# Optimization experiments

Measured on AMD Instinct MI355X. Metric: run time of the kernel, lower is better.

The kernel has to match this reference:

```python
import jax, jax.numpy as jnp
import numpy as np
import math

V, T, D, H, L, B = 50257, 1024, 768, 12, 6, 2
FF = 4 * D
HD = D // H

def layernorm(x, g, b, eps=1e-5):
    mu = jnp.mean(x, axis=-1, keepdims=True)
    var = jnp.var(x, axis=-1, keepdims=True)
    return (x - mu) * jax.lax.rsqrt(var + eps) * g + b

def new_gelu(x):
    # Faithful to the (buggy) NewGelu: tanh arg = sqrt(2/pi) * 0.044715 * x**4
    c = math.sqrt(2.0 / math.pi)
    return 0.5 * x * (1.0 + jnp.tanh(c * (x * 0.044715 * jnp.power(x, 3))))

def setup_inputs() -> dict:
    key = jax.random.key(0)
    ks = jax.random.split(key, 18)
    n = lambda k, shape, s=0.02: (jax.random.normal(k, shape, dtype=jnp.float32) * s)
    return {
        "ids": jax.random.randint(ks[0], (B, T), 0, V),
        "wte": n(ks[1], (V, D)),
        "wpe": n(ks[2], (T, D)),
        "W_qkv": n(ks[3], (L, D, 3 * D)),
        "b_qkv": jnp.zeros((L, 3 * D), jnp.float32),
        "W_o": n(ks[4], (L, D, D)),
        "b_o": jnp.zeros((L, D), jnp.float32),
        "ln1_g": jnp.ones((L, D), jnp.float32),
        "ln1_b": jnp.zeros((L, D), jnp.float32),
        "W1": n(ks[5], (L, D, FF)),
        "b1": jnp.zeros((L, FF), jnp.float32),
        "W2": n(ks[6], (L, FF, D)),
        "b2": jnp.zeros((L, D), jnp.float32),
        "lnf_g": jnp.ones((D,), jnp.float32),
        "lnf_b": jnp.zeros((D,), jnp.float32),
        "W_head": n(ks[7], (D, V)),
        "b_head": jnp.zeros((V,), jnp.float32),
    }

def reference(ids, wte, wpe, W_qkv, b_qkv, W_o, b_o, ln1_g, ln1_b,
              W1, b1, W2, b2, lnf_g, lnf_b, W_head, b_head):
    t = ids.shape[1]
    x = wte[ids] + wpe[:t][None]  # [B,T,D]
    scale = 1.0 / math.sqrt(HD)
    for l in range(L):
        qkv = x @ W_qkv[l] + b_qkv[l]                 # [B,T,3D]
        q, k, v = jnp.split(qkv, 3, axis=-1)
        q = q.reshape(-1, t, H, HD).transpose(0, 2, 1, 3)  # [B,H,T,hd]
        k = k.reshape(-1, t, H, HD).transpose(0, 2, 1, 3)
        v = v.reshape(-1, t, H, HD).transpose(0, 2, 1, 3)
        # NOTE: mask buffer is all-ones in the source, so NO causal masking.
        att = jax.nn.softmax(jnp.einsum('bhqd,bhkd->bhqk', q, k) * scale, axis=-1)
        y = jnp.einsum('bhqk,bhkd->bhqd', att, v)
        y = y.transpose(0, 2, 1, 3).reshape(-1, t, D)
        y = y @ W_o[l] + b_o[l]
        x = layernorm(y, ln1_g[l], ln1_b[l]) + x      # ln1 AFTER attn, per source
        h = new_gelu(x @ W1[l] + b1[l]) @ W2[l] + b2[l]  # ln2 unused, per source
        x = h + x
    x = layernorm(x, lnf_g, lnf_b)
    logits = x @ W_head + b_head
    return logits
```

## Files before the change

kernel.cpp:

```cpp
#include <hip/hip_runtime.h>
#include <hip/hip_bf16.h>
#include <math.h>
#include <stdint.h>

#define NL 6
#define NB 2
#define ST 1024
#define ND 768
#define NH 12
#define HD 64
#define NFF 3072
#define NV 50257
#define ND3 2304
#define NM (NB * ST)

typedef short bf16x4 __attribute__((ext_vector_type(4)));
typedef short bf16x8 __attribute__((ext_vector_type(8)));
typedef float f32x4  __attribute__((ext_vector_type(4)));

typedef __attribute__((address_space(3))) void as3_void;
typedef __attribute__((address_space(1))) void as1_void;

__device__ __forceinline__ void async_copy16(const void* g, void* lds) {
  __builtin_amdgcn_global_load_lds((const as1_void*)(uintptr_t)g,
                                   (as3_void*)(uint32_t)(uintptr_t)lds,
                                   16, 0, 0);
}

__device__ __forceinline__ unsigned short f2bf(float f) {
  union { float f; uint32_t u; } v; v.f = f;
  return (unsigned short)((v.u + 0x7fffu + ((v.u >> 16) & 1u)) >> 16);
}

__device__ __forceinline__ bf16x8 frag16(const unsigned short* p) {
  return *(const bf16x8*)p;
}

template <int N>
__device__ __forceinline__ void wait_vm_barrier() {
  if constexpr (N == 8)      asm volatile("s_waitcnt vmcnt(8)\n\ts_barrier" ::: "memory");
  else if constexpr (N == 6) asm volatile("s_waitcnt vmcnt(6)\n\ts_barrier" ::: "memory");
  else if constexpr (N == 4) asm volatile("s_waitcnt vmcnt(4)\n\ts_barrier" ::: "memory");
  else                       asm volatile("s_waitcnt vmcnt(0)\n\ts_barrier" ::: "memory");
}
__device__ __forceinline__ void lgkm_barrier() {
  asm volatile("s_waitcnt lgkmcnt(0)\n\ts_barrier" ::: "memory");
}

#define MFMA(a, b, c) __builtin_amdgcn_mfma_f32_16x16x32_bf16((a), (b), (c), 0, 0, 0)

__device__ __forceinline__ float gelu_buggy(float x) {
  const float c = 0.7978845608028654f;
  float x2 = x * x;
  return 0.5f * x * (1.0f + tanhf(c * 0.044715f * x2 * x2));
}

enum { EP_QKV = 0, EP_PROJ, EP_FF1, EP_FF2, EP_HEAD };

template <int EPI, int TM, int TN, int WN, int NW, int BK>
__global__ __launch_bounds__(NW * 64)
void gemm_bt(const unsigned short* __restrict__ A,
             const unsigned short* __restrict__ BT,
             const float* __restrict__ bias,
             float* __restrict__ Cf,
             unsigned short* __restrict__ Cb,
             const float* __restrict__ resid,
             unsigned short* __restrict__ vT,
             int M, int N, int K)
{
  constexpr int WM = NW / WN;
  constexpr int FM = TM / WM / 16;
  constexpr int FN = TN / WN / 16;
  constexpr int SL = BK / 8;
  constexpr int RS = (BK == 32) ? 1 : 0;
  constexpr int RPC = 1024 / (BK * 2);
  constexpr int CA = TM / RPC / NW;
  constexpr int CB = TN / RPC / NW;
  constexpr int LPT = CA + CB;
  constexpr int KK = BK / 32;
  __shared__ __align__(16) unsigned short As[2][TM * BK];
  __shared__ __align__(16) unsigned short Bs[2][TN * BK];
  const int tid = threadIdx.x;
  const int w = tid >> 6, l = tid & 63;
  const int g = l >> 4, r = l & 15;
  const int wm = (w / WN) * (FM * 16);
  const int wn = (w % WN) * (FN * 16);

  const int nbx = gridDim.x;
  const int nwg = nbx * gridDim.y;
  int bid = blockIdx.y * nbx + blockIdx.x;
  if ((nwg & 7) == 0) bid = (bid & 7) * (nwg >> 3) + (bid >> 3);
  const int m0 = (bid % nbx) * TM, n0 = (bid / nbx) * TN;

  const int sr = l / (BK / 8);
  const int se = ((l & (SL - 1)) ^ ((sr >> RS) & (SL - 1))) * 8;
  long aoff[CA];
  long boff[CB];
#pragma unroll
  for (int c = 0; c < CA; ++c) {
    const int arow = (w * CA + c) * RPC + sr;
    aoff[c] = (long)(m0 + arow) * K + se;
  }
#pragma unroll
  for (int c = 0; c < CB; ++c) {
    int brow = n0 + (w * CB + c) * RPC + sr;
    if (brow > N - 1) brow = N - 1;
    boff[c] = (long)brow * K + se;
  }

  f32x4 acc[FM][FN] = {};

  auto stage = [&](int t, int buf) {
    const long k0 = (long)t * BK;
#pragma unroll
    for (int c = 0; c < CA; ++c)
      async_copy16(A + aoff[c] + k0, &As[buf][(w * CA + c) * 512]);
#pragma unroll
    for (int c = 0; c < CB; ++c)
      async_copy16(BT + boff[c] + k0, &Bs[buf][(w * CB + c) * 512]);
  };

  auto compute = [&](int buf) {
#pragma unroll
    for (int kk = 0; kk < KK; ++kk) {
      bf16x8 af[FM], bf[FN];
#pragma unroll
      for (int mi = 0; mi < FM; ++mi)
        af[mi] = frag16(&As[buf][(wm + mi * 16 + r) * BK +
                                 (((kk * 4 + g) ^ ((r >> RS) & (SL - 1))) * 8)]);
#pragma unroll
      for (int ni = 0; ni < FN; ++ni)
        bf[ni] = frag16(&Bs[buf][(wn + ni * 16 + r) * BK +
                                 (((kk * 4 + g) ^ ((r >> RS) & (SL - 1))) * 8)]);
      __builtin_amdgcn_s_setprio(1);
#pragma unroll
      for (int mi = 0; mi < FM; ++mi)
#pragma unroll
        for (int ni = 0; ni < FN; ++ni)
          acc[mi][ni] = MFMA(af[mi], bf[ni], acc[mi][ni]);
      __builtin_amdgcn_s_setprio(0);
    }
  };

  const int nt = K / BK;
  stage(0, 0);
  for (int t = 0; t < nt - 1; ++t) {
    stage(t + 1, (t + 1) & 1);
    wait_vm_barrier<LPT>();
    compute(t & 1);
    lgkm_barrier();
  }
  wait_vm_barrier<0>();
  compute((nt - 1) & 1);

#pragma unroll
  for (int mi = 0; mi < FM; ++mi) {
#pragma unroll
    for (int ni = 0; ni < FN; ++ni) {
      const int col = n0 + wn + ni * 16 + r;
      if (EPI == EP_HEAD && col >= N) continue;
      const float bb = bias[col];
      if (EPI == EP_QKV && col >= 2 * ND) {
        const int hv = (col - 2 * ND) >> 6, d = (col - 2 * ND) & 63;
        short4 vv;
#pragma unroll
        for (int q = 0; q < 4; ++q)
          vv[q] = (short)f2bf(acc[mi][ni][q] + bb);
        const int row = m0 + wm + mi * 16 + g * 4;
        const int bb_ = row >> 10, t4 = row & 1023;
        *(short4*)&vT[(((long)bb_ * NH + hv) * HD + d) * ST + t4] = vv;
        continue;
      }
#pragma unroll
      for (int q = 0; q < 4; ++q) {
        const int row = m0 + wm + mi * 16 + g * 4 + q;
        float v = acc[mi][ni][q] + bb;
        if constexpr (EPI == EP_QKV) {
          Cb[(long)row * N + col] = f2bf(v);
        } else if constexpr (EPI == EP_PROJ) {
          Cf[(long)row * N + col] = v;
        } else if constexpr (EPI == EP_FF1) {
          Cb[(long)row * N + col] = f2bf(gelu_buggy(v));
        } else if constexpr (EPI == EP_FF2) {
          float o = v + resid[(long)row * N + col];
          Cf[(long)row * N + col] = o;
          Cb[(long)row * N + col] = f2bf(o);
        } else {
          Cf[(long)row * N + col] = v;
        }
      }
    }
  }
}

__global__ __launch_bounds__(256)
void attn_kernel(const unsigned short* __restrict__ qkv,
                 const unsigned short* __restrict__ vT,
                 unsigned short* __restrict__ y)
{
  constexpr int LS = 72;
  __shared__ __align__(16) unsigned short Qs[64 * LS];
  __shared__ __align__(16) unsigned short Ks[64 * LS];
  __shared__ __align__(16) unsigned short Vt[64 * LS];
  __shared__ __align__(16) unsigned short Ps[64 * LS];
  const int tid = threadIdx.x;
  const int w = tid >> 6, l = tid & 63;
  const int g = l >> 4, r = l & 15;
  const int q0 = blockIdx.x * 64;
  const int b = blockIdx.y / NH, h = blockIdx.y % NH;
  const long rb = (long)b * ST;
  const long vbase = ((long)b * NH + h) * HD * ST;
  const int srow = tid >> 3, sc8 = (tid & 7) * 8;

#pragma unroll
  for (int p = 0; p < 2; ++p) {
    const int row = p * 32 + srow;
    bf16x8 v = *(const bf16x8*)&qkv[(rb + q0 + row) * ND3 + h * HD + sc8];
    *(bf16x8*)&Qs[row * LS + sc8] = v;
  }
  __syncthreads();
  bf16x8 aq[2];
#pragma unroll
  for (int kk = 0; kk < 2; ++kk)
    aq[kk] = *(const bf16x8*)&Qs[(w * 16 + r) * LS + kk * 32 + g * 8];

  float m_run[4] = {-1e30f, -1e30f, -1e30f, -1e30f};
  float l_run[4] = {0.f, 0.f, 0.f, 0.f};
  f32x4 acc_o[4] = {};

  for (int kt = 0; kt < ST / 64; ++kt) {
#pragma unroll
    for (int p = 0; p < 2; ++p) {
      const int row = p * 32 + srow;
      *(bf16x8*)&Ks[row * LS + sc8] =
          *(const bf16x8*)&qkv[(rb + kt * 64 + row) * ND3 + ND + h * HD + sc8];
      *(bf16x8*)&Vt[row * LS + sc8] =
          *(const bf16x8*)&vT[vbase + (long)row * ST + kt * 64 + sc8];
    }
    __syncthreads();

    f32x4 s_acc[4] = {};
#pragma unroll
    for (int kk = 0; kk < 2; ++kk) {
#pragma unroll
      for (int ni = 0; ni < 4; ++ni) {
        bf16x8 bk = *(const bf16x8*)&Ks[(ni * 16 + r) * LS + kk * 32 + g * 8];
        s_acc[ni] = MFMA(aq[kk], bk, s_acc[ni]);
      }
    }

    float mloc[4];
#pragma unroll
    for (int q = 0; q < 4; ++q) {
      float mx = fmaxf(fmaxf(s_acc[0][q], s_acc[1][q]), fmaxf(s_acc[2][q], s_acc[3][q]));
      mloc[q] = mx * 0.125f;
    }
#pragma unroll
    for (int mask = 1; mask < 16; mask <<= 1)
#pragma unroll
      for (int q = 0; q < 4; ++q)
        mloc[q] = fmaxf(mloc[q], __shfl_xor(mloc[q], mask, 64));

    float alpha[4], psum[4] = {0.f, 0.f, 0.f, 0.f};
#pragma unroll
    for (int q = 0; q < 4; ++q) {
      const float mn = fmaxf(m_run[q], mloc[q]);
      alpha[q] = __expf(m_run[q] - mn);
      m_run[q] = mn;
    }
#pragma unroll
    for (int ni = 0; ni < 4; ++ni)
#pragma unroll
      for (int q = 0; q < 4; ++q) {
        const float p = __expf(s_acc[ni][q] * 0.125f - m_run[q]);
        psum[q] += p;
        Ps[(w * 16 + g * 4 + q) * LS + ni * 16 + r] = f2bf(p);
      }
#pragma unroll
    for (int mask = 1; mask < 16; mask <<= 1)
#pragma unroll
      for (int q = 0; q < 4; ++q) psum[q] += __shfl_xor(psum[q], mask, 64);
#pragma unroll
    for (int q = 0; q < 4; ++q) l_run[q] = l_run[q] * alpha[q] + psum[q];
#pragma unroll
    for (int ni = 0; ni < 4; ++ni)
#pragma unroll
      for (int q = 0; q < 4; ++q) acc_o[ni][q] *= alpha[q];

    asm volatile("s_waitcnt lgkmcnt(0)" ::: "memory");
    __builtin_amdgcn_sched_barrier(0);

#pragma unroll
    for (int kk = 0; kk < 2; ++kk) {
      bf16x8 ap = *(const bf16x8*)&Ps[(w * 16 + r) * LS + kk * 32 + g * 8];
#pragma unroll
      for (int ni = 0; ni < 4; ++ni) {
        bf16x8 bv = *(const bf16x8*)&Vt[(ni * 16 + r) * LS + kk * 32 + g * 8];
        acc_o[ni] = MFMA(ap, bv, acc_o[ni]);
      }
    }
    __syncthreads();
  }

#pragma unroll
  for (int ni = 0; ni < 4; ++ni)
#pragma unroll
    for (int q = 0; q < 4; ++q) {
      const int row = q0 + w * 16 + g * 4 + q;
      const int col = h * HD + ni * 16 + r;
      y[(rb + row) * ND + col] = f2bf(acc_o[ni][q] / l_run[q]);
    }
}

template <bool RESID>
__global__ __launch_bounds__(256)
void ln_kernel(const float* __restrict__ in, const float* __restrict__ resid,
               const float* __restrict__ gamma, const float* __restrict__ beta,
               float* __restrict__ out_f, unsigned short* __restrict__ out_b)
{
  __shared__ float wred[8];
  const int row = blockIdx.x, tid = threadIdx.x;
  float v[3];
#pragma unroll
  for (int j = 0; j < 3; ++j) v[j] = in[(long)row * ND + tid + j * 256];
  float s = v[0] + v[1] + v[2];
#pragma unroll
  for (int m = 1; m < 64; m <<= 1) s += __shfl_xor(s, m, 64);
  if ((tid & 63) == 0) wred[tid >> 6] = s;
  __syncthreads();
  const float mean = (wred[0] + wred[1] + wred[2] + wred[3]) * (1.0f / ND);
  float d[3];
#pragma unroll
  for (int j = 0; j < 3; ++j) d[j] = v[j] - mean;
  float s2 = d[0] * d[0] + d[1] * d[1] + d[2] * d[2];
#pragma unroll
  for (int m = 1; m < 64; m <<= 1) s2 += __shfl_xor(s2, m, 64);
  if ((tid & 63) == 0) wred[4 + (tid >> 6)] = s2;
  __syncthreads();
  const float var = (wred[4] + wred[5] + wred[6] + wred[7]) * (1.0f / ND);
  const float rstd = rsqrtf(var + 1e-5f);
#pragma unroll
  for (int j = 0; j < 3; ++j) {
    const int c = tid + j * 256;
    float o = d[j] * rstd * gamma[c] + beta[c];
    if (RESID) o += resid[(long)row * ND + c];
    if (out_f) out_f[(long)row * ND + c] = o;
    if (out_b) out_b[(long)row * ND + c] = f2bf(o);
  }
}

__global__ __launch_bounds__(256)
void embed_kernel(const int* __restrict__ ids, const float* __restrict__ wte,
                  const float* __restrict__ wpe, float* __restrict__ x,
                  unsigned short* __restrict__ xb)
{
  const int t = blockIdx.x, tid = threadIdx.x;
  const int tok = ids[t];
  const int pos = t & (ST - 1);
#pragma unroll
  for (int j = 0; j < 3; ++j) {
    const int c = tid + j * 256;
    const float v = wte[(long)tok * ND + c] + wpe[(long)pos * ND + c];
    x[(long)t * ND + c] = v;
    xb[(long)t * ND + c] = f2bf(v);
  }
}

__global__ __launch_bounds__(256)
void transpose_bf16(const float* __restrict__ in, unsigned short* __restrict__ out,
                    int R, int C)
{
  __shared__ float tile[64][33];
  const long z = (long)blockIdx.z * R * C;
  const int c0 = blockIdx.x * 32, r0 = blockIdx.y * 64;
  const int tx = threadIdx.x & 31, ty = threadIdx.x >> 5;
#pragma unroll
  for (int j = 0; j < 8; ++j) {
    const int rr = r0 + j * 8 + ty, cc = c0 + tx;
    if (cc < C) tile[j * 8 + ty][tx] = in[z + (long)rr * C + cc];
  }
  __syncthreads();
  const int rx = threadIdx.x & 63, cy = threadIdx.x >> 6;
#pragma unroll
  for (int j = 0; j < 8; ++j) {
    const int cc = c0 + j * 4 + cy;
    if (cc < C) out[z + (long)cc * R + r0 + rx] = f2bf(tile[rx][j * 4 + cy]);
  }
}

extern "C" void kernel_launch(void* const* d_in, const int* in_sizes, int n_in,
                              void* d_out, int out_size, void* d_ws, size_t ws_size,
                              hipStream_t stream)
{
  const int*   ids    = (const int*)d_in[0];
  const float* wte    = (const float*)d_in[1];
  const float* wpe    = (const float*)d_in[2];
  const float* W_qkv  = (const float*)d_in[3];
  const float* b_qkv  = (const float*)d_in[4];
  const float* W_o    = (const float*)d_in[5];
  const float* b_o    = (const float*)d_in[6];
  const float* ln1_g  = (const float*)d_in[7];
  const float* ln1_b  = (const float*)d_in[8];
  const float* W1     = (const float*)d_in[9];
  const float* b1     = (const float*)d_in[10];
  const float* W2     = (const float*)d_in[11];
  const float* b2     = (const float*)d_in[12];
  const float* lnf_g  = (const float*)d_in[13];
  const float* lnf_b  = (const float*)d_in[14];
  const float* W_head = (const float*)d_in[15];
  const float* b_head = (const float*)d_in[16];
  float* out = (float*)d_out;
  (void)in_sizes; (void)n_in; (void)out_size; (void)ws_size;

  char* ws = (char*)d_ws;
  size_t off = 0;
  auto alloc = [&](size_t bytes) -> void* {
    void* p = (void*)(ws + off);
    off = (off + bytes + 255) & ~(size_t)255;
    return p;
  };
  unsigned short* wqkvT = (unsigned short*)alloc((size_t)NL * ND3 * ND * 2);
  unsigned short* woT   = (unsigned short*)alloc((size_t)NL * ND * ND * 2);
  unsigned short* w1T   = (unsigned short*)alloc((size_t)NL * NFF * ND * 2);
  unsigned short* w2T   = (unsigned short*)alloc((size_t)NL * ND * NFF * 2);
  unsigned short* whT   = (unsigned short*)alloc((size_t)NV * ND * 2);
  float*          xf    = (float*)alloc((size_t)NM * ND * 4);
  unsigned short* xb    = (unsigned short*)alloc((size_t)NM * ND * 2);
  unsigned short* qkvb  = (unsigned short*)alloc((size_t)NM * ND3 * 2);
  unsigned short* yb    = (unsigned short*)alloc((size_t)NM * ND * 2);
  float*          aof   = (float*)alloc((size_t)NM * ND * 4);
  unsigned short* h1b   = (unsigned short*)alloc((size_t)NM * NFF * 2);
  unsigned short* xlnb  = (unsigned short*)alloc((size_t)NM * ND * 2);
  unsigned short* vtb   = (unsigned short*)alloc((size_t)NB * NH * HD * ST * 2);

  dim3 tb(256);
  dim3 tb128(128);
  dim3 tb512(512);
  transpose_bf16<<<dim3(ND3 / 32, ND / 64, NL), tb, 0, stream>>>(W_qkv, wqkvT, ND, ND3);
  transpose_bf16<<<dim3(ND / 32, ND / 64, NL), tb, 0, stream>>>(W_o, woT, ND, ND);
  transpose_bf16<<<dim3(NFF / 32, ND / 64, NL), tb, 0, stream>>>(W1, w1T, ND, NFF);
  transpose_bf16<<<dim3(ND / 32, NFF / 64, NL), tb, 0, stream>>>(W2, w2T, NFF, ND);
  transpose_bf16<<<dim3((NV + 31) / 32, ND / 64, 1), tb, 0, stream>>>(W_head, whT, ND, NV);

  embed_kernel<<<dim3(NM), tb, 0, stream>>>(ids, wte, wpe, xf, xb);

  for (int l = 0; l < NL; ++l) {
    gemm_bt<EP_QKV, 128, 128, 2, 4, 64><<<dim3(NM / 128, ND3 / 128), tb, 0, stream>>>(
        xb, wqkvT + (size_t)l * ND3 * ND, b_qkv + (size_t)l * ND3,
        nullptr, qkvb, nullptr, vtb, NM, ND3, ND);
    attn_kernel<<<dim3(ST / 64, NB * NH), tb, 0, stream>>>(qkvb, vtb, yb);
    gemm_bt<EP_PROJ, 64, 64, 2, 2, 64><<<dim3(NM / 64, ND / 64), tb128, 0, stream>>>(
        yb, woT + (size_t)l * ND * ND, b_o + (size_t)l * ND,
        aof, nullptr, nullptr, nullptr, NM, ND, ND);
    ln_kernel<true><<<dim3(NM), tb, 0, stream>>>(
        aof, xf, ln1_g + (size_t)l * ND, ln1_b + (size_t)l * ND, xf, xb);
    gemm_bt<EP_FF1, 128, 128, 2, 4, 64><<<dim3(NM / 128, NFF / 128), tb, 0, stream>>>(
        xb, w1T + (size_t)l * NFF * ND, b1 + (size_t)l * NFF,
        nullptr, h1b, nullptr, nullptr, NM, NFF, ND);
    gemm_bt<EP_FF2, 64, 64, 2, 2, 64><<<dim3(NM / 64, ND / 64), tb128, 0, stream>>>(
        h1b, w2T + (size_t)l * ND * NFF, b2 + (size_t)l * ND,
        xf, xb, xf, nullptr, NM, ND, NFF);
  }
  ln_kernel<false><<<dim3(NM), tb, 0, stream>>>(xf, nullptr, lnf_g, lnf_b, nullptr, xlnb);
  gemm_bt<EP_HEAD, 256, 256, 4, 8, 32><<<dim3(NM / 256, (NV + 255) / 256), tb512, 0, stream>>>(
      xlnb, whT, b_head, out, nullptr, nullptr, nullptr, NM, NV, ND);
}
```

Baseline: 1.155 ms.

## Add configurable multi-buffer GEMM pipeline; triple-buffer head, narrow QKV/FF1 tiles

```diff
diff --git a/kernel.cpp b/kernel.cpp
--- a/kernel.cpp
+++ b/kernel.cpp
@@ -57,7 +57,7 @@
 
 enum { EP_QKV = 0, EP_PROJ, EP_FF1, EP_FF2, EP_HEAD };
 
-template <int EPI, int TM, int TN, int WN, int NW, int BK>
+template <int EPI, int TM, int TN, int WN, int NW, int BK, int NBUF>
 __global__ __launch_bounds__(NW * 64)
 void gemm_bt(const unsigned short* __restrict__ A,
              const unsigned short* __restrict__ BT,
@@ -78,8 +78,9 @@
   constexpr int CB = TN / RPC / NW;
   constexpr int LPT = CA + CB;
   constexpr int KK = BK / 32;
-  __shared__ __align__(16) unsigned short As[2][TM * BK];
-  __shared__ __align__(16) unsigned short Bs[2][TN * BK];
+  constexpr int DEPTH = NBUF - 1;
+  __shared__ __align__(16) unsigned short As[NBUF][TM * BK];
+  __shared__ __align__(16) unsigned short Bs[NBUF][TN * BK];
   const int tid = threadIdx.x;
   const int w = tid >> 6, l = tid & 63;
   const int g = l >> 4, r = l & 15;
@@ -144,14 +145,19 @@
 
   const int nt = K / BK;
   stage(0, 0);
-  for (int t = 0; t < nt - 1; ++t) {
-    stage(t + 1, (t + 1) & 1);
-    wait_vm_barrier<LPT>();
-    compute(t & 1);
-    lgkm_barrier();
-  }
-  wait_vm_barrier<0>();
-  compute((nt - 1) & 1);
+  if (DEPTH == 2) stage(1, 1);
+  int cur = 0, nxt = DEPTH;
+  for (int t = 0; t < nt; ++t) {
+    const bool have_next = (t + DEPTH) < nt;
+    if (have_next) stage(t + DEPTH, nxt);
+    if (have_next && DEPTH == 2)       wait_vm_barrier<2 * LPT>();
+    else if (have_next || (DEPTH == 2 && t + 1 < nt)) wait_vm_barrier<LPT>();
+    else                               wait_vm_barrier<0>();
+    compute(cur);
+    if (t + 1 < nt) lgkm_barrier();
+    cur = (cur + 1 == NBUF) ? 0 : cur + 1;
+    nxt = (nxt + 1 == NBUF) ? 0 : nxt + 1;
+  }
 
 #pragma unroll
   for (int mi = 0; mi < FM; ++mi) {
@@ -445,23 +451,23 @@
   embed_kernel<<<dim3(NM), tb, 0, stream>>>(ids, wte, wpe, xf, xb);
 
   for (int l = 0; l < NL; ++l) {
-    gemm_bt<EP_QKV, 128, 128, 2, 4, 64><<<dim3(NM / 128, ND3 / 128), tb, 0, stream>>>(
+    gemm_bt<EP_QKV, 128, 64, 2, 4, 64, 2><<<dim3(NM / 128, ND3 / 64), tb, 0, stream>>>(
         xb, wqkvT + (size_t)l * ND3 * ND, b_qkv + (size_t)l * ND3,
         nullptr, qkvb, nullptr, vtb, NM, ND3, ND);
     attn_kernel<<<dim3(ST / 64, NB * NH), tb, 0, stream>>>(qkvb, vtb, yb);
-    gemm_bt<EP_PROJ, 64, 64, 2, 2, 64><<<dim3(NM / 64, ND / 64), tb128, 0, stream>>>(
+    gemm_bt<EP_PROJ, 64, 64, 2, 2, 64, 2><<<dim3(NM / 64, ND / 64), tb128, 0, stream>>>(
         yb, woT + (size_t)l * ND * ND, b_o + (size_t)l * ND,
         aof, nullptr, nullptr, nullptr, NM, ND, ND);
     ln_kernel<true><<<dim3(NM), tb, 0, stream>>>(
         aof, xf, ln1_g + (size_t)l * ND, ln1_b + (size_t)l * ND, xf, xb);
-    gemm_bt<EP_FF1, 128, 128, 2, 4, 64><<<dim3(NM / 128, NFF / 128), tb, 0, stream>>>(
+    gemm_bt<EP_FF1, 128, 64, 2, 4, 64, 2><<<dim3(NM / 128, NFF / 64), tb, 0, stream>>>(
         xb, w1T + (size_t)l * NFF * ND, b1 + (size_t)l * NFF,
         nullptr, h1b, nullptr, nullptr, NM, NFF, ND);
-    gemm_bt<EP_FF2, 64, 64, 2, 2, 64><<<dim3(NM / 64, ND / 64), tb128, 0, stream>>>(
+    gemm_bt<EP_FF2, 64, 64, 2, 2, 64, 2><<<dim3(NM / 64, ND / 64), tb128, 0, stream>>>(
         h1b, w2T + (size_t)l * ND * NFF, b2 + (size_t)l * ND,
         xf, xb, xf, nullptr, NM, ND, NFF);
   }
   ln_kernel<false><<<dim3(NM), tb, 0, stream>>>(xf, nullptr, lnf_g, lnf_b, nullptr, xlnb);
-  gemm_bt<EP_HEAD, 256, 256, 4, 8, 32><<<dim3(NM / 256, (NV + 255) / 256), tb512, 0, stream>>>(
+  gemm_bt<EP_HEAD, 256, 256, 4, 8, 32, 3><<<dim3(NM / 256, (NV + 255) / 256), tb512, 0, stream>>>(
       xlnb, whT, b_head, out, nullptr, nullptr, nullptr, NM, NV, ND);
 }
```

Measured after the change: 1.132 ms. 1.02x faster.
